# Optimization experiments

Measured on AMD Instinct MI355X. Metric: run time of the kernel, lower is better.

The kernel has to match this reference:

```python
import jax, jax.numpy as jnp
import numpy as np

NUM_HEADS = 16
HEAD_DIM = 64
MAX_POS = 2048  # max_position_embeddings


def setup_inputs() -> dict:
    key = jax.random.key(0)
    ks = jax.random.split(key, 8)
    B, S, H = 4, 1024, 1024
    s = 1.0 / np.sqrt(H)
    return {
        "hidden_states": jax.random.normal(ks[0], (B, S, H), jnp.float32),
        "attention_mask": jnp.zeros((B, 1, 1, S), jnp.float32),
        "Wq": jax.random.normal(ks[1], (H, H), jnp.float32) * s,
        "bq": jnp.zeros((H,), jnp.float32),
        "Wk": jax.random.normal(ks[2], (H, H), jnp.float32) * s,
        "bk": jnp.zeros((H,), jnp.float32),
        "Wv": jax.random.normal(ks[3], (H, H), jnp.float32) * s,
        "bv": jnp.zeros((H,), jnp.float32),
        "dist_emb": jax.random.normal(ks[4], (2 * MAX_POS - 1, HEAD_DIM), jnp.float32) * 0.02,
    }


def _split_heads(x):
    B, S, _ = x.shape
    return x.reshape(B, S, NUM_HEADS, HEAD_DIM).transpose(0, 2, 1, 3)  # [B,H,S,dh]


def reference(hidden_states, attention_mask, Wq, bq, Wk, bk, Wv, bv, dist_emb):
    B, S, _ = hidden_states.shape
    q = _split_heads(hidden_states @ Wq + bq)
    k = _split_heads(hidden_states @ Wk + bk)
    v = _split_heads(hidden_states @ Wv + bv)

    scores = jnp.einsum("bhld,bhrd->bhlr", q, k)

    # relative_key_query positional bias
    pos = jnp.arange(S)
    distance = pos[:, None] - pos[None, :]                 # [S,S]
    pe = dist_emb[distance + MAX_POS - 1]                   # [S,S,dh]
    scores = scores + jnp.einsum("bhld,lrd->bhlr", q, pe)
    scores = scores + jnp.einsum("bhrd,lrd->bhlr", k, pe)

    scores = scores / np.sqrt(HEAD_DIM).astype(np.float32)
    scores = scores + attention_mask                        # additive mask broadcast
    probs = jax.nn.softmax(scores, axis=-1)                 # dropout is identity in eval

    ctx = jnp.einsum("bhlr,bhrd->bhld", probs, v)
    ctx = ctx.transpose(0, 2, 1, 3).reshape(B, S, NUM_HEADS * HEAD_DIM)
    return ctx
```

## Files before the change

### kernel.cpp

```cpp
#include <hip/hip_runtime.h>
#include <hip/hip_bf16.h>

typedef __hip_bfloat16 bf16;
typedef __attribute__((ext_vector_type(8))) short bf16x8;
typedef __attribute__((ext_vector_type(4))) float f32x4;
typedef __attribute__((ext_vector_type(2))) unsigned int u32x2;

#define MFMA(a, b, c) __builtin_amdgcn_mfma_f32_16x16x32_bf16((a), (b), (c), 0, 0, 0)

static __device__ __forceinline__ float bf2f(bf16 b) { return __bfloat162float(b); }

static __device__ __forceinline__ unsigned pk2(float a, float b) {
    return __builtin_amdgcn_perm(__builtin_bit_cast(unsigned, b),
                                 __builtin_bit_cast(unsigned, a), 0x07060302u);
}

static __device__ __forceinline__ float quad_max(float x) {
    x = fmaxf(x, __shfl_xor(x, 16));
    x = fmaxf(x, __shfl_xor(x, 32));
    return x;
}
static __device__ __forceinline__ float quad_sum(float x) {
    x += __shfl_xor(x, 16);
    x += __shfl_xor(x, 32);
    return x;
}

__global__ void prep_convert(const float* __restrict__ X, const float* __restrict__ DE,
                             bf16* __restrict__ Xb, bf16* __restrict__ DEb) {
    int i = blockIdx.x * blockDim.x + threadIdx.x;
    if (i < 1048576) {
        float4 v = reinterpret_cast<const float4*>(X)[i];
        bf16* d = Xb + 4 * i;
        d[0] = __float2bfloat16(v.x); d[1] = __float2bfloat16(v.y);
        d[2] = __float2bfloat16(v.z); d[3] = __float2bfloat16(v.w);
    } else {
        int j = i - 1048576;
        if (j < 65520) {
            float4 v = reinterpret_cast<const float4*>(DE)[j];
            bf16* d = DEb + 4 * j;
            d[0] = __float2bfloat16(v.x); d[1] = __float2bfloat16(v.y);
            d[2] = __float2bfloat16(v.z); d[3] = __float2bfloat16(v.w);
        }
    }
}

__global__ void prep_transpose_w(const float* __restrict__ Wq, const float* __restrict__ Wk,
                                 const float* __restrict__ Wv, bf16* __restrict__ WTb) {
    const float* W = (blockIdx.z == 0) ? Wq : (blockIdx.z == 1) ? Wk : Wv;
    bf16* WT = WTb + (size_t)blockIdx.z * (1024u * 1024u);
    __shared__ float t[64][65];
    int tid = threadIdx.x;
    int col = tid & 63;
    int r4 = tid >> 6;
    int i0 = blockIdx.x * 64, o0 = blockIdx.y * 64;
    for (int it = 0; it < 16; ++it) {
        int row = it * 4 + r4;
        t[row][col] = W[(size_t)(i0 + row) * 1024 + o0 + col];
    }
    __syncthreads();
    for (int it = 0; it < 16; ++it) {
        int row = it * 4 + r4;
        WT[(size_t)(o0 + row) * 1024 + i0 + col] = __float2bfloat16(t[col][row]);
    }
}

__global__ __launch_bounds__(256, 2) void proj_gemm(
    const bf16* __restrict__ Xb, const bf16* __restrict__ WTb,
    const float* __restrict__ bq, const float* __restrict__ bk, const float* __restrict__ bv,
    bf16* __restrict__ Qb, bf16* __restrict__ Kb, bf16* __restrict__ VTb) {
    int proj = blockIdx.z;
    const bf16* W = WTb + (size_t)proj * (1024u * 1024u);
    const float* bias = (proj == 0) ? bq : (proj == 1) ? bk : bv;

    __shared__ bf16 XT[128][72];
    __shared__ bf16 WTt[128][72];

    int tid = threadIdx.x;
    int w = tid >> 6, lane = tid & 63, g = lane >> 4, li = lane & 15;
    int wr = w >> 1, wc = w & 1;
    int m0 = blockIdx.x * 128, n0 = blockIdx.y * 128;

    f32x4 acc[4][4];
    for (int mt = 0; mt < 4; mt++)
        for (int nt = 0; nt < 4; nt++) acc[mt][nt] = {0.f, 0.f, 0.f, 0.f};

    for (int ks = 0; ks < 16; ++ks) {
        for (int it = 0; it < 4; ++it) {
            int idx = tid + 256 * it;
            int row = idx >> 3, c = (idx & 7) * 8;
            *reinterpret_cast<bf16x8*>(&XT[row][c]) =
                *reinterpret_cast<const bf16x8*>(Xb + (size_t)(m0 + row) * 1024 + ks * 64 + c);
            *reinterpret_cast<bf16x8*>(&WTt[row][c]) =
                *reinterpret_cast<const bf16x8*>(W + (size_t)(n0 + row) * 1024 + ks * 64 + c);
        }
        __syncthreads();
        for (int kk = 0; kk < 2; ++kk) {
            bf16x8 af[4], bfr[4];
            for (int mt = 0; mt < 4; mt++)
                af[mt] = *reinterpret_cast<const bf16x8*>(&XT[64 * wr + 16 * mt + li][32 * kk + 8 * g]);
            for (int nt = 0; nt < 4; nt++)
                bfr[nt] = *reinterpret_cast<const bf16x8*>(&WTt[64 * wc + 16 * nt + li][32 * kk + 8 * g]);
            for (int mt = 0; mt < 4; mt++)
                for (int nt = 0; nt < 4; nt++)
                    acc[mt][nt] = MFMA(af[mt], bfr[nt], acc[mt][nt]);
        }
        __syncthreads();
    }

    for (int mt = 0; mt < 4; mt++)
        for (int nt = 0; nt < 4; nt++) {
            int n = n0 + 64 * wc + 16 * nt + li;
            int h = n >> 6, d = n & 63;
            float bv_ = bias[n];
            for (int r = 0; r < 4; r++) {
                int m = m0 + 64 * wr + 16 * mt + 4 * g + r;
                int b = m >> 10, s = m & 1023;
                bf16 o = __float2bfloat16(acc[mt][nt][r] + bv_);
                if (proj == 0)      Qb[((size_t)(b * 16 + h) * 1024 + s) * 64 + d] = o;
                else if (proj == 1) Kb[((size_t)(b * 16 + h) * 1024 + s) * 64 + d] = o;
                else                VTb[((size_t)(b * 16 + h) * 64 + d) * 1024 + s] = o;
            }
        }
}

__global__ __launch_bounds__(256, 2) void attn_fused(
    const bf16* __restrict__ Qg, const bf16* __restrict__ Kg,
    const bf16* __restrict__ VTg, const bf16* __restrict__ DEb,
    const float* __restrict__ mask, float* __restrict__ out) {
    const int S = 1024, D = 64;
    const float C8 = 0.18033688011112042f;
    int p_ = blockIdx.x;
    int bh = (p_ & 7) * 8 + ((p_ >> 3) >> 4);
    int qb = (p_ >> 3) & 15;
    int b = bh >> 4, h = bh & 15;
    int L0 = qb * 64;

    int tid = threadIdx.x;
    int w = tid >> 6, lane = tid & 63, g = lane >> 4, li = lane & 15;

    __shared__ __align__(16) char smem[78336];
    bf16 (*K_lds)[72]      = reinterpret_cast<bf16(*)[72]>(smem);
    bf16 (*VT_lds)[64][72] = reinterpret_cast<bf16(*)[64][72]>(smem + 9216);
    bf16 (*DE_lds)[72]     = reinterpret_cast<bf16(*)[72]>(smem + 27648);
    float (*M_lds)[64] = reinterpret_cast<float(*)[64]>(smem + 77824);

    const bf16* Qh = Qg + (size_t)bh * S * D;
    const bf16* Kh = Kg + (size_t)bh * S * D;
    const bf16* Vh = VTg + (size_t)bh * D * S;
    const float* maskb = mask + (size_t)b * S;

    int srow = tid >> 3;
    int scol = (tid & 7) * 8;

    bf16x8 qa0, qa1;
    {
        const bf16* qrow = Qh + (size_t)(L0 + 16 * w + li) * D;
        qa0 = *reinterpret_cast<const bf16x8*>(qrow + 8 * g);
        qa1 = *reinterpret_cast<const bf16x8*>(qrow + 32 + 8 * g);
    }

    const char* qdb = smem + 46080 + 2816 * w + 178 * li - 8 * g;
    const char* kdb = smem + 57344 + 664 * g + 32 * w + 2 * li + 30;
    char* qsp = smem + 46080 + 2816 * w + 176 * li + 8 * g;
    char* ksp = smem + 57344 + 168 * (48 - 16 * w + li) + 8 * g;
    char* Pp = smem + 68608 + 2304 * w + 144 * li;

    int de00 = L0 + 1984;
    {
        for (int c = 0; c < 2; ++c) {
            int row = srow + 32 * c;
            *reinterpret_cast<bf16x8*>(&K_lds[row][scol]) =
                *reinterpret_cast<const bf16x8*>(Kh + (size_t)row * D + scol);
            *reinterpret_cast<bf16x8*>(&VT_lds[0][row][scol]) =
                *reinterpret_cast<const bf16x8*>(Vh + (size_t)row * S + scol);
        }
        for (int c = 0; c < 4; ++c) {
            int j = srow + 32 * c;
            *reinterpret_cast<bf16x8*>(&DE_lds[(de00 + j) & 127][scol]) =
                *reinterpret_cast<const bf16x8*>(DEb + (size_t)(de00 + j) * 64 + scol);
        }
        if (tid < 64) M_lds[0][tid] = maskb[tid];
    }

    f32x4 acc_o[4];
    for (int dt = 0; dt < 4; dt++) acc_o[dt] = {0.f, 0.f, 0.f, 0.f};
    float m_run = -1e30f, l_run = 0.f;

    __syncthreads();

    for (int kt = 0; kt < 16; ++kt) {
        int r0 = kt * 64;
        int de0 = de00 - r0;
        bool has_next = (kt < 15);

        bf16x8 sK0, sK1, sV0, sV1, sD0, sD1;
        float sM;
        if (has_next) {
            int r0n = r0 + 64;
            int dlo = de0 - 64;
            sK0 = *reinterpret_cast<const bf16x8*>(Kh + (size_t)(r0n + srow) * D + scol);
            sK1 = *reinterpret_cast<const bf16x8*>(Kh + (size_t)(r0n + srow + 32) * D + scol);
            sV0 = *reinterpret_cast<const bf16x8*>(Vh + (size_t)srow * S + r0n + scol);
            sV1 = *reinterpret_cast<const bf16x8*>(Vh + (size_t)(srow + 32) * S + r0n + scol);
            sD0 = *reinterpret_cast<const bf16x8*>(DEb + (size_t)(dlo + srow) * 64 + scol);
            sD1 = *reinterpret_cast<const bf16x8*>(DEb + (size_t)(dlo + srow + 32) * 64 + scol);
            if (tid < 64) sM = maskb[r0n + tid];
        }

        __builtin_amdgcn_s_setprio(1);
        f32x4 s_acc[4];
        #pragma unroll
        for (int nt = 0; nt < 4; ++nt) {
            bf16x8 kb0 = *reinterpret_cast<const bf16x8*>(&K_lds[16 * nt + li][8 * g]);
            bf16x8 kb1 = *reinterpret_cast<const bf16x8*>(&K_lds[16 * nt + li][32 + 8 * g]);
            f32x4 z = {0.f, 0.f, 0.f, 0.f};
            z = MFMA(kb0, qa0, z);
            z = MFMA(kb1, qa1, z);
            s_acc[nt] = z;
        }
        {
            int kr = 16 * (3 - w) + li;
            bf16x8 ka0 = *reinterpret_cast<const bf16x8*>(&K_lds[kr][8 * g]);
            bf16x8 ka1 = *reinterpret_cast<const bf16x8*>(&K_lds[kr][32 + 8 * g]);
            #pragma unroll
            for (int jt = 0; jt < 5; ++jt) {
                int dr = (de0 + 16 * w + 16 * jt + li) & 127;
                bf16x8 d0 = *reinterpret_cast<const bf16x8*>(&DE_lds[dr][8 * g]);
                bf16x8 d1 = *reinterpret_cast<const bf16x8*>(&DE_lds[dr][32 + 8 * g]);
                f32x4 aq = {0.f, 0.f, 0.f, 0.f};
                aq = MFMA(d0, qa0, aq);
                aq = MFMA(d1, qa1, aq);
                f32x4 ak = {0.f, 0.f, 0.f, 0.f};
                ak = MFMA(d0, ka0, ak);
                ak = MFMA(d1, ka1, ak);
                u32x2 uq = {pk2(aq[0], aq[1]), pk2(aq[2], aq[3])};
                *reinterpret_cast<u32x2*>(qsp + 32 * jt) = uq;
                u32x2 uk = {pk2(ak[0], ak[1]), pk2(ak[2], ak[3])};
                *reinterpret_cast<u32x2*>(ksp + 32 * jt) = uk;
            }
        }
        __builtin_amdgcn_s_setprio(0);
        __syncthreads();

        float u[4][4];
        float lmax = -1e30f;
        #pragma unroll
        for (int nt = 0; nt < 4; ++nt) {
            f32x4 mk4 = *reinterpret_cast<const f32x4*>(&M_lds[kt & 1][16 * nt + 4 * g]);
            #pragma unroll
            for (int r = 0; r < 4; ++r) {
                float qd = bf2f(*reinterpret_cast<const bf16*>(qdb + (126 - 32 * nt - 2 * r)));
                float kd = bf2f(*reinterpret_cast<const bf16*>(kdb + (2688 * nt + 166 * r)));
                float uu = s_acc[nt][r] + qd + kd;
                uu = __builtin_fmaf(mk4[r], 8.0f, uu);
                u[nt][r] = uu;
                lmax = fmaxf(lmax, uu);
            }
        }
        float tm = quad_max(lmax);
        bool noskip = !__all(tm <= m_run);
        float scl = 1.0f;
        if (noskip) {
            float mnew = fmaxf(m_run, tm);
            scl = exp2f((m_run - mnew) * C8);
            m_run = mnew;
        }
        float nmc = -m_run * C8;
        float pv[4][4];
        #pragma unroll
        for (int nt = 0; nt < 4; ++nt)
            #pragma unroll
            for (int r = 0; r < 4; ++r)
                pv[nt][r] = exp2f(__builtin_fmaf(u[nt][r], C8, nmc));
        float t0 = (pv[0][0] + pv[0][1]) + (pv[0][2] + pv[0][3]);
        float t1 = (pv[1][0] + pv[1][1]) + (pv[1][2] + pv[1][3]);
        float t2 = (pv[2][0] + pv[2][1]) + (pv[2][2] + pv[2][3]);
        float t3 = (pv[3][0] + pv[3][1]) + (pv[3][2] + pv[3][3]);
        float qs = quad_sum((t0 + t1) + (t2 + t3));
        if (noskip) {
            l_run = l_run * scl + qs;
            #pragma unroll
            for (int dt = 0; dt < 4; dt++) acc_o[dt] *= scl;
        } else {
            l_run += qs;
        }

        #pragma unroll
        for (int nt = 0; nt < 4; ++nt) {
            u32x2 pp = {pk2(pv[nt][0], pv[nt][1]), pk2(pv[nt][2], pv[nt][3])};
            *reinterpret_cast<u32x2*>(Pp + 32 * nt + 8 * g) = pp;
        }
        bf16x8 pb0 = *reinterpret_cast<const bf16x8*>(Pp + 16 * g);
        bf16x8 pb1 = *reinterpret_cast<const bf16x8*>(Pp + 64 + 16 * g);

        __builtin_amdgcn_s_setprio(1);
        #pragma unroll
        for (int dt = 0; dt < 4; dt++) {
            bf16x8 va0 = *reinterpret_cast<const bf16x8*>(&VT_lds[kt & 1][16 * dt + li][8 * g]);
            bf16x8 va1 = *reinterpret_cast<const bf16x8*>(&VT_lds[kt & 1][16 * dt + li][32 + 8 * g]);
            acc_o[dt] = MFMA(va0, pb0, acc_o[dt]);
            acc_o[dt] = MFMA(va1, pb1, acc_o[dt]);
        }
        __builtin_amdgcn_s_setprio(0);

        if (has_next) {
            int dlo = de0 - 64;
            *reinterpret_cast<bf16x8*>(&K_lds[srow][scol]) = sK0;
            *reinterpret_cast<bf16x8*>(&K_lds[srow + 32][scol]) = sK1;
            *reinterpret_cast<bf16x8*>(&VT_lds[(kt + 1) & 1][srow][scol]) = sV0;
            *reinterpret_cast<bf16x8*>(&VT_lds[(kt + 1) & 1][srow + 32][scol]) = sV1;
            *reinterpret_cast<bf16x8*>(&DE_lds[(dlo + srow) & 127][scol]) = sD0;
            *reinterpret_cast<bf16x8*>(&DE_lds[(dlo + srow + 32) & 127][scol]) = sD1;
            if (tid < 64) M_lds[(kt + 1) & 1][tid] = sM;
        }
        __syncthreads();
    }

    float inv = 1.0f / l_run;
    float (*OT)[68] = reinterpret_cast<float (*)[68]>(smem + 27648);
    #pragma unroll
    for (int dt = 0; dt < 4; dt++)
        #pragma unroll
        for (int r = 0; r < 4; r++)
            OT[16 * w + li][16 * dt + 4 * g + r] = acc_o[dt][r] * inv;
    __syncthreads();
    {
        int q = tid >> 2, seg = tid & 3;
        float* gout = out + ((size_t)(b * 1024 + L0 + q)) * 1024 + h * 64 + 16 * seg;
        #pragma unroll
        for (int j = 0; j < 4; ++j)
            *reinterpret_cast<float4*>(gout + 4 * j) =
                *reinterpret_cast<const float4*>(&OT[q][16 * seg + 4 * j]);
    }
}

extern "C" void kernel_launch(void* const* d_in, const int* in_sizes, int n_in,
                              void* d_out, int out_size, void* d_ws, size_t ws_size,
                              hipStream_t stream) {
    const float* X   = (const float*)d_in[0];
    const float* msk = (const float*)d_in[1];
    const float* Wq  = (const float*)d_in[2];
    const float* bq  = (const float*)d_in[3];
    const float* Wk  = (const float*)d_in[4];
    const float* bk  = (const float*)d_in[5];
    const float* Wv  = (const float*)d_in[6];
    const float* bv  = (const float*)d_in[7];
    const float* DE  = (const float*)d_in[8];
    float* out = (float*)d_out;

    bf16* ws  = (bf16*)d_ws;
    bf16* Xb  = ws;
    bf16* WTb = ws + 4194304;
    bf16* DEb = ws + 7340032;
    bf16* Qb  = ws + 7602176;
    bf16* Kb  = ws + 11796480;
    bf16* VTb = ws + 15990784;

    prep_convert<<<4352, 256, 0, stream>>>(X, DE, Xb, DEb);
    prep_transpose_w<<<dim3(16, 16, 3), 256, 0, stream>>>(Wq, Wk, Wv, WTb);
    proj_gemm<<<dim3(32, 8, 3), 256, 0, stream>>>(Xb, WTb, bq, bk, bv, Qb, Kb, VTb);
    attn_fused<<<dim3(1024), 256, 0, stream>>>(Qb, Kb, VTb, DEb, msk, out);
}
```

Before: 160.7 us.

## Load K/V/DE tiles directly to LDS with global_load_lds and XOR swizzle

```diff
diff --git a/kernel.cpp b/kernel.cpp
--- a/kernel.cpp
+++ b/kernel.cpp
@@ -13,6 +13,12 @@
 static __device__ __forceinline__ unsigned pk2(float a, float b) {
     return __builtin_amdgcn_perm(__builtin_bit_cast(unsigned, b),
                                  __builtin_bit_cast(unsigned, a), 0x07060302u);
+}
+
+static __device__ __forceinline__ void gload16(const void* g, void* l) {
+    __builtin_amdgcn_global_load_lds(
+        (const __attribute__((address_space(1))) void*)g,
+        (__attribute__((address_space(3))) void*)l, 16, 0, 0);
 }
 
 static __device__ __forceinline__ float quad_max(float x) {
@@ -139,19 +145,24 @@
     int tid = threadIdx.x;
     int w = tid >> 6, lane = tid & 63, g = lane >> 4, li = lane & 15;
 
-    __shared__ __align__(16) char smem[78336];
-    bf16 (*K_lds)[72]      = reinterpret_cast<bf16(*)[72]>(smem);
-    bf16 (*VT_lds)[64][72] = reinterpret_cast<bf16(*)[64][72]>(smem + 9216);
-    bf16 (*DE_lds)[72]     = reinterpret_cast<bf16(*)[72]>(smem + 27648);
-    float (*M_lds)[64] = reinterpret_cast<float(*)[64]>(smem + 77824);
+    __shared__ __align__(16) char smem[72704];
+    float (*M_lds)[64] = reinterpret_cast<float(*)[64]>(smem + 72192);
 
     const bf16* Qh = Qg + (size_t)bh * S * D;
     const bf16* Kh = Kg + (size_t)bh * S * D;
     const bf16* Vh = VTg + (size_t)bh * D * S;
     const float* maskb = mask + (size_t)b * S;
 
-    int srow = tid >> 3;
-    int scol = (tid & 7) * 8;
+    int sw = (li & 7) << 4;
+    int c0 = (16 * g) ^ sw;
+    int c1 = (64 + 16 * g) ^ sw;
+    const char* KbL = smem + li * 128;
+    const char* KaL = smem + (16 * (3 - w) + li) * 128;
+    const char* Vb_ = smem + 8192 + li * 128;
+    const char* Db_ = smem + 24576;
+
+    int cr = lane >> 3;
+    int sc = 16 * ((lane & 7) ^ cr);
 
     bf16x8 qa0, qa1;
     {
@@ -160,25 +171,27 @@
         qa1 = *reinterpret_cast<const bf16x8*>(qrow + 32 + 8 * g);
     }
 
-    const char* qdb = smem + 46080 + 2816 * w + 178 * li - 8 * g;
-    const char* kdb = smem + 57344 + 664 * g + 32 * w + 2 * li + 30;
-    char* qsp = smem + 46080 + 2816 * w + 176 * li + 8 * g;
-    char* ksp = smem + 57344 + 168 * (48 - 16 * w + li) + 8 * g;
-    char* Pp = smem + 68608 + 2304 * w + 144 * li;
+    const char* qdb = smem + 40960 + 2816 * w + 178 * li - 8 * g;
+    const char* kdb = smem + 52224 + 664 * g + 32 * w + 2 * li + 30;
+    char* qsp = smem + 40960 + 2816 * w + 176 * li + 8 * g;
+    char* ksp = smem + 52224 + 168 * (48 - 16 * w + li) + 8 * g;
+    char* Pp  = smem + 62976 + 2304 * w + 144 * li;
 
     int de00 = L0 + 1984;
     {
-        for (int c = 0; c < 2; ++c) {
-            int row = srow + 32 * c;
-            *reinterpret_cast<bf16x8*>(&K_lds[row][scol]) =
-                *reinterpret_cast<const bf16x8*>(Kh + (size_t)row * D + scol);
-            *reinterpret_cast<bf16x8*>(&VT_lds[0][row][scol]) =
-                *reinterpret_cast<const bf16x8*>(Vh + (size_t)row * S + scol);
-        }
-        for (int c = 0; c < 4; ++c) {
-            int j = srow + 32 * c;
-            *reinterpret_cast<bf16x8*>(&DE_lds[(de00 + j) & 127][scol]) =
-                *reinterpret_cast<const bf16x8*>(DEb + (size_t)(de00 + j) * 64 + scol);
+        #pragma unroll
+        for (int i = 0; i < 2; ++i) {
+            int blk = w * 2 + i;
+            int row = blk * 8 + cr;
+            gload16((const char*)Kh + (size_t)row * 128 + sc, smem + blk * 1024);
+            gload16((const char*)Vh + (size_t)row * 2048 + sc, smem + 8192 + blk * 1024);
+        }
+        #pragma unroll
+        for (int i = 0; i < 4; ++i) {
+            int blk = w * 4 + i;
+            int row = blk * 8 + cr;
+            int ldsoff = (((de00 & 64) * 128) + blk * 1024) & 16383;
+            gload16((const char*)DEb + (size_t)(de00 + row) * 128 + sc, smem + 24576 + ldsoff);
         }
         if (tid < 64) M_lds[0][tid] = maskb[tid];
     }
@@ -194,40 +207,25 @@
         int de0 = de00 - r0;
         bool has_next = (kt < 15);
 
-        bf16x8 sK0, sK1, sV0, sV1, sD0, sD1;
-        float sM;
-        if (has_next) {
-            int r0n = r0 + 64;
-            int dlo = de0 - 64;
-            sK0 = *reinterpret_cast<const bf16x8*>(Kh + (size_t)(r0n + srow) * D + scol);
-            sK1 = *reinterpret_cast<const bf16x8*>(Kh + (size_t)(r0n + srow + 32) * D + scol);
-            sV0 = *reinterpret_cast<const bf16x8*>(Vh + (size_t)srow * S + r0n + scol);
-            sV1 = *reinterpret_cast<const bf16x8*>(Vh + (size_t)(srow + 32) * S + r0n + scol);
-            sD0 = *reinterpret_cast<const bf16x8*>(DEb + (size_t)(dlo + srow) * 64 + scol);
-            sD1 = *reinterpret_cast<const bf16x8*>(DEb + (size_t)(dlo + srow + 32) * 64 + scol);
-            if (tid < 64) sM = maskb[r0n + tid];
-        }
-
         __builtin_amdgcn_s_setprio(1);
         f32x4 s_acc[4];
         #pragma unroll
         for (int nt = 0; nt < 4; ++nt) {
-            bf16x8 kb0 = *reinterpret_cast<const bf16x8*>(&K_lds[16 * nt + li][8 * g]);
-            bf16x8 kb1 = *reinterpret_cast<const bf16x8*>(&K_lds[16 * nt + li][32 + 8 * g]);
+            bf16x8 kb0 = *reinterpret_cast<const bf16x8*>(KbL + nt * 2048 + c0);
+            bf16x8 kb1 = *reinterpret_cast<const bf16x8*>(KbL + nt * 2048 + c1);
             f32x4 z = {0.f, 0.f, 0.f, 0.f};
             z = MFMA(kb0, qa0, z);
             z = MFMA(kb1, qa1, z);
             s_acc[nt] = z;
         }
         {
-            int kr = 16 * (3 - w) + li;
-            bf16x8 ka0 = *reinterpret_cast<const bf16x8*>(&K_lds[kr][8 * g]);
-            bf16x8 ka1 = *reinterpret_cast<const bf16x8*>(&K_lds[kr][32 + 8 * g]);
+            bf16x8 ka0 = *reinterpret_cast<const bf16x8*>(KaL + c0);
+            bf16x8 ka1 = *reinterpret_cast<const bf16x8*>(KaL + c1);
             #pragma unroll
             for (int jt = 0; jt < 5; ++jt) {
                 int dr = (de0 + 16 * w + 16 * jt + li) & 127;
-                bf16x8 d0 = *reinterpret_cast<const bf16x8*>(&DE_lds[dr][8 * g]);
-                bf16x8 d1 = *reinterpret_cast<const bf16x8*>(&DE_lds[dr][32 + 8 * g]);
+                bf16x8 d0 = *reinterpret_cast<const bf16x8*>(Db_ + dr * 128 + c0);
+                bf16x8 d1 = *reinterpret_cast<const bf16x8*>(Db_ + dr * 128 + c1);
                 f32x4 aq = {0.f, 0.f, 0.f, 0.f};
                 aq = MFMA(d0, qa0, aq);
                 aq = MFMA(d1, qa1, aq);
@@ -243,6 +241,23 @@
         __builtin_amdgcn_s_setprio(0);
         __syncthreads();
 
+        float sM;
+        if (has_next) {
+            int r0n = r0 + 64;
+            int dlo = de0 - 64;
+            #pragma unroll
+            for (int i = 0; i < 2; ++i) {
+                int blk = w * 2 + i;
+                int row = blk * 8 + cr;
+                gload16((const char*)Kh + (size_t)(r0n + row) * 128 + sc, smem + blk * 1024);
+                gload16((const char*)Vh + (size_t)row * 2048 + (size_t)r0n * 2 + sc,
+                        smem + 8192 + ((kt + 1) & 1) * 8192 + blk * 1024);
+                gload16((const char*)DEb + (size_t)(dlo + row) * 128 + sc,
+                        smem + 24576 + (dlo & 64) * 128 + blk * 1024);
+            }
+            if (tid < 64) sM = maskb[r0n + tid];
+        }
+
         float u[4][4];
         float lmax = -1e30f;
         #pragma unroll
@@ -295,30 +310,22 @@
         bf16x8 pb1 = *reinterpret_cast<const bf16x8*>(Pp + 64 + 16 * g);
 
         __builtin_amdgcn_s_setprio(1);
+        const char* Vt = Vb_ + (kt & 1) * 8192;
         #pragma unroll
         for (int dt = 0; dt < 4; dt++) {
-            bf16x8 va0 = *reinterpret_cast<const bf16x8*>(&VT_lds[kt & 1][16 * dt + li][8 * g]);
-            bf16x8 va1 = *reinterpret_cast<const bf16x8*>(&VT_lds[kt & 1][16 * dt + li][32 + 8 * g]);
+            bf16x8 va0 = *reinterpret_cast<const bf16x8*>(Vt + dt * 2048 + c0);
+            bf16x8 va1 = *reinterpret_cast<const bf16x8*>(Vt + dt * 2048 + c1);
             acc_o[dt] = MFMA(va0, pb0, acc_o[dt]);
             acc_o[dt] = MFMA(va1, pb1, acc_o[dt]);
         }
         __builtin_amdgcn_s_setprio(0);
 
-        if (has_next) {
-            int dlo = de0 - 64;
-            *reinterpret_cast<bf16x8*>(&K_lds[srow][scol]) = sK0;
-            *reinterpret_cast<bf16x8*>(&K_lds[srow + 32][scol]) = sK1;
-            *reinterpret_cast<bf16x8*>(&VT_lds[(kt + 1) & 1][srow][scol]) = sV0;
-            *reinterpret_cast<bf16x8*>(&VT_lds[(kt + 1) & 1][srow + 32][scol]) = sV1;
-            *reinterpret_cast<bf16x8*>(&DE_lds[(dlo + srow) & 127][scol]) = sD0;
-            *reinterpret_cast<bf16x8*>(&DE_lds[(dlo + srow + 32) & 127][scol]) = sD1;
-            if (tid < 64) M_lds[(kt + 1) & 1][tid] = sM;
-        }
+        if (has_next && tid < 64) M_lds[(kt + 1) & 1][tid] = sM;
         __syncthreads();
     }
 
     float inv = 1.0f / l_run;
-    float (*OT)[68] = reinterpret_cast<float (*)[68]>(smem + 27648);
+    float (*OT)[68] = reinterpret_cast<float (*)[68]>(smem);
     #pragma unroll
     for (int dt = 0; dt < 4; dt++)
         #pragma unroll
```

After: 152.5 us. 1.05x faster.
